# Kernel optimization log

Hardware: AMD Instinct MI355X
Metric: run time of the kernel (lower is better)

Reference implementation:

```python
import jax, jax.numpy as jnp
import numpy as np

B, T, H = 128, 1024, 512


def setup_inputs() -> dict:
    key = jax.random.key(0)
    ks = jax.random.split(key, 4)
    vel = jax.random.normal(ks[0], (B, T, 2), dtype=jnp.float32)
    # weight_ih ~ N(0, sqrt(1/2)); weight_hh orthogonal; biases zero; output zeroed
    # (we use random output weights so fwd output is non-trivial for testing)
    W_ih = jax.random.normal(ks[1], (H, 2), dtype=jnp.float32) * np.sqrt(0.5)
    A = jax.random.normal(ks[2], (H, H), dtype=jnp.float32)
    Q, _ = jnp.linalg.qr(A)
    W_hh = Q.astype(jnp.float32)
    b_ih = jnp.zeros((H,), dtype=jnp.float32)
    b_hh = jnp.zeros((H,), dtype=jnp.float32)
    W_out = jax.random.normal(ks[3], (2, H), dtype=jnp.float32) * 0.05
    b_out = jnp.zeros((2,), dtype=jnp.float32)
    return {"vel": vel, "W_ih": W_ih, "W_hh": W_hh, "b_ih": b_ih,
            "b_hh": b_hh, "W_out": W_out, "b_out": b_out}


def reference(vel, W_ih, W_hh, b_ih, b_hh, W_out, b_out):
    # Precompute input projection for all timesteps: [B, T, H]
    x_proj = jnp.einsum('btc,hc->bth', vel, W_ih) + b_ih + b_hh
    x_tbh = jnp.swapaxes(x_proj, 0, 1)  # [T, B, H] for scan over time

    def step(h, x_t):
        # h: [B, H]; x_t: [B, H]
        h_new = jnp.tanh(x_t + h @ W_hh.T)
        return h_new, h_new

    h0 = jnp.zeros((vel.shape[0], W_hh.shape[0]), dtype=vel.dtype)
    _, u_tbh = jax.lax.scan(step, h0, x_tbh)
    u_vals = jnp.swapaxes(u_tbh, 0, 1)  # [B, T, H]
    pos_est = jnp.einsum('bth,oh->bto', u_vals, W_out) + b_out  # [B, T, 2]
    return pos_est, u_vals
```

## Files before the change

kernel.cpp:

```cpp
#include <hip/hip_runtime.h>
#include <hip/hip_bf16.h>


#define TT 1024
#define BB 128
#define HH 512

typedef short s16x8 __attribute__((ext_vector_type(8)));
typedef float f32x4 __attribute__((ext_vector_type(4)));
typedef unsigned int uint;
typedef unsigned short ushort_t;
typedef unsigned long long u64;

#define MFMA_B16(a, b, c) __builtin_amdgcn_mfma_f32_16x16x32_bf16((a), (b), (c), 0, 0, 0)
#define ALD(p) __hip_atomic_load((p), __ATOMIC_RELAXED, __HIP_MEMORY_SCOPE_AGENT)
#define AST(p, v) __hip_atomic_store((p), (v), __ATOMIC_RELAXED, __HIP_MEMORY_SCOPE_AGENT)

static __device__ __forceinline__ ushort_t bf16_rne(float f) {
  uint u = __float_as_uint(f);
  u += 0x7fffu + ((u >> 16) & 1u);
  return (ushort_t)(u >> 16);
}

static __device__ __forceinline__ float tanh_fast(float z) {
  float e = __expf(2.0f * z);
  return 1.0f - 2.0f * __builtin_amdgcn_rcpf(e + 1.0f);
}

static __device__ __forceinline__ s16x8 packW(const float* wp) {
  float4 lo = *(const float4*)wp;
  float4 hi = *(const float4*)(wp + 4);
  s16x8 s;
  s[0] = (short)bf16_rne(lo.x); s[1] = (short)bf16_rne(lo.y);
  s[2] = (short)bf16_rne(lo.z); s[3] = (short)bf16_rne(lo.w);
  s[4] = (short)bf16_rne(hi.x); s[5] = (short)bf16_rne(hi.y);
  s[6] = (short)bf16_rne(hi.z); s[7] = (short)bf16_rne(hi.w);
  return s;
}

__global__ __launch_bounds__(256) void rnn_kernel(
    const float* __restrict__ vel, const float* __restrict__ W_ih,
    const float* __restrict__ W_hh, const float* __restrict__ b_ih,
    const float* __restrict__ b_hh, float* __restrict__ u_out,
    u64* __restrict__ pub) {
  __shared__ uint4 hlds_mem[2048];
  char* hlds = (char*)hlds_mem;

  const int tid = threadIdx.x;
  const int lane = tid & 63;
  const int w = tid >> 6;
  const int c = blockIdx.x & 7;
  const int p = blockIdx.x >> 3;
  const int l15 = lane & 15;
  const int kg = lane >> 4;
  const int n0 = p * 128 + w * 32;
  const uint swz = ((uint)l15 & 7u) << 4;

  s16x8 wl[2][4], wr[2][12];
#pragma unroll
  for (int nt = 0; nt < 2; ++nt) {
    const float* wb = W_hh + (size_t)(n0 + nt * 16 + l15) * HH + kg * 8;
#pragma unroll
    for (int kk = 0; kk < 4; ++kk)
      wl[nt][kk] = packW(wb + (p * 4 + kk) * 32);
#pragma unroll
    for (int j = 0; j < 12; ++j)
      wr[nt][j] = packW(wb + (((p * 4 + 4 + j) & 15)) * 32);
  }
  float wih0[2], wih1[2], bs[2];
#pragma unroll
  for (int nt = 0; nt < 2; ++nt) {
    int n = n0 + nt * 16 + l15;
    wih0[nt] = W_ih[n * 2 + 0];
    wih1[nt] = W_ih[n * 2 + 1];
    bs[nt] = b_ih[n] + b_hh[n];
  }

  {
    uint4 z = {0u, 0u, 0u, 0u};
    uint4* zp = (uint4*)(hlds + tid * 64);
    zp[0] = z; zp[1] = z; zp[2] = z; zp[3] = z;
  }
  __syncthreads();

  const f32x4 z4 = {0.f, 0.f, 0.f, 0.f};
  const int ps0 = (p + 1) & 3, ps1 = (p + 2) & 3, ps2 = (p + 3) & 3;
  const uint remoff = (uint)(p * 256 + 256);

  for (int t = 0; t < TT; ++t) {
    const int cur = t & 1;
    const int nxt = cur ^ 1;

    u64 g00 = 0, g01 = 0, g02 = 0, g03 = 0;
    u64 g10 = 0, g11 = 0, g12 = 0, g13 = 0;
    u64 g20 = 0, g21 = 0, g22 = 0, g23 = 0;
    const u64* sp0 = pub + ((size_t)(cur * 8 + c) * 4 + ps0) * 1024 + tid * 4;
    const u64* sp1 = pub + ((size_t)(cur * 8 + c) * 4 + ps1) * 1024 + tid * 4;
    const u64* sp2 = pub + ((size_t)(cur * 8 + c) * 4 + ps2) * 1024 + tid * 4;
    if (t > 0) {
      g00 = ALD(sp0); g01 = ALD(sp0 + 1); g02 = ALD(sp0 + 2); g03 = ALD(sp0 + 3);
      g10 = ALD(sp1); g11 = ALD(sp1 + 1); g12 = ALD(sp1 + 2); g13 = ALD(sp1 + 3);
      g20 = ALD(sp2); g21 = ALD(sp2 + 1); g22 = ALD(sp2 + 2); g23 = ALD(sp2 + 3);
      asm volatile("" ::: "memory");
    }

    float2 v[4];
#pragma unroll
    for (int r = 0; r < 4; ++r)
      v[r] = *(const float2*)(vel + ((size_t)(c * 16 + kg * 4 + r) * TT + t) * 2);

    f32x4 a00 = z4, a01 = z4, a10 = z4, a11 = z4;
    const uint abase = (uint)cur * 16384u + (uint)l15 * 1024u + (uint)kg * 16u;
#pragma unroll
    for (int kk = 0; kk < 4; ++kk) {
      s16x8 f = *(const s16x8*)(hlds + ((abase + (uint)(p * 256 + kk * 64)) ^ swz));
      if (kk & 1) { a01 = MFMA_B16(f, wl[0][kk], a01); a11 = MFMA_B16(f, wl[1][kk], a11); }
      else        { a00 = MFMA_B16(f, wl[0][kk], a00); a10 = MFMA_B16(f, wl[1][kk], a10); }
    }

    if (t > 0) {
      const uint tgt = (uint)t;
      const uint grow = (uint)tid >> 4;
      const uint gb = ((uint)cur * 16384u + grow * 1024u + (((uint)tid << 2) & 63u) * 4u) ^
                      ((grow & 7u) << 4);
      while (true) {
        uint mn = min(min((uint)(g00 >> 32), (uint)(g01 >> 32)),
                      min((uint)(g02 >> 32), (uint)(g03 >> 32)));
        if (mn >= tgt) break;
        g00 = ALD(sp0); g01 = ALD(sp0 + 1); g02 = ALD(sp0 + 2); g03 = ALD(sp0 + 3);
      }
      { uint4 d = {(uint)g00, (uint)g01, (uint)g02, (uint)g03};
        *(uint4*)(hlds + (gb ^ ((uint)ps0 * 256u))) = d; }
      while (true) {
        uint mn = min(min((uint)(g10 >> 32), (uint)(g11 >> 32)),
                      min((uint)(g12 >> 32), (uint)(g13 >> 32)));
        if (mn >= tgt) break;
        g10 = ALD(sp1); g11 = ALD(sp1 + 1); g12 = ALD(sp1 + 2); g13 = ALD(sp1 + 3);
      }
      { uint4 d = {(uint)g10, (uint)g11, (uint)g12, (uint)g13};
        *(uint4*)(hlds + (gb ^ ((uint)ps1 * 256u))) = d; }
      while (true) {
        uint mn = min(min((uint)(g20 >> 32), (uint)(g21 >> 32)),
                      min((uint)(g22 >> 32), (uint)(g23 >> 32)));
        if (mn >= tgt) break;
        g20 = ALD(sp2); g21 = ALD(sp2 + 1); g22 = ALD(sp2 + 2); g23 = ALD(sp2 + 3);
      }
      { uint4 d = {(uint)g20, (uint)g21, (uint)g22, (uint)g23};
        *(uint4*)(hlds + (gb ^ ((uint)ps2 * 256u))) = d; }
      __syncthreads();
    }

#pragma unroll
    for (int j = 0; j < 12; ++j) {
      uint off = (remoff + (uint)(j * 64)) & 1023u;
      s16x8 f = *(const s16x8*)(hlds + ((abase + off) ^ swz));
      if (j & 1) { a01 = MFMA_B16(f, wr[0][j], a01); a11 = MFMA_B16(f, wr[1][j], a11); }
      else       { a00 = MFMA_B16(f, wr[0][j], a00); a10 = MFMA_B16(f, wr[1][j], a10); }
    }
    f32x4 acc0 = a00 + a01;
    f32x4 acc1 = a10 + a11;

    float uv0[4], uv1[4];
    ushort_t hb0[4], hb1[4];
#pragma unroll
    for (int r = 0; r < 4; ++r) {
      float x0 = fmaf(v[r].x, wih0[0], fmaf(v[r].y, wih1[0], bs[0]));
      float x1 = fmaf(v[r].x, wih0[1], fmaf(v[r].y, wih1[1], bs[1]));
      uv0[r] = tanh_fast(x0 + acc0[r]);
      uv1[r] = tanh_fast(x1 + acc1[r]);
      hb0[r] = bf16_rne(uv0[r]);
      hb1[r] = bf16_rne(uv1[r]);
    }

    if (t < TT - 1) {
      const bool odd = (l15 & 1) != 0;
      const uint rowbase = (uint)(kg * 4) + (odd ? 2u : 0u);
      const uint cpq = (uint)(w * 16) + ((uint)l15 >> 1);
      u64* dpb = pub + ((size_t)(nxt * 8 + c) * 4 + p) * 1024;
      const u64 tagw = (u64)(uint)(t + 1) << 32;
      const uint ldsb = (uint)nxt * 16384u;
#pragma unroll
      for (int nt = 0; nt < 2; ++nt) {
        const ushort_t* hb = nt ? hb1 : hb0;
        uint a01p = (uint)hb[0] | ((uint)hb[1] << 16);
        uint a23p = (uint)hb[2] | ((uint)hb[3] << 16);
        uint b01p = __shfl_xor(a01p, 1);
        uint b23p = __shfl_xor(a23p, 1);
        uint eP = odd ? b23p : a01p;
        uint oP = odd ? a23p : b01p;
        uint pr0 = (eP & 0xFFFFu) | (oP << 16);
        uint pr1 = (eP >> 16) | (oP & 0xFFFF0000u);
        uint cp = cpq + (uint)(nt * 8);
        AST(dpb + rowbase * 64 + cp, (u64)pr0 | tagw);
        AST(dpb + (rowbase + 1) * 64 + cp, (u64)pr1 | tagw);
        uint cb = (uint)(n0 + nt * 16 + (l15 & ~1)) * 2u;
        *(uint*)(hlds + ((ldsb + rowbase * 1024u + cb) ^ ((rowbase & 7u) << 4))) = pr0;
        *(uint*)(hlds + ((ldsb + (rowbase + 1) * 1024u + cb) ^ (((rowbase + 1) & 7u) << 4))) = pr1;
      }
    }

#pragma unroll
    for (int r = 0; r < 4; ++r) {
      size_t ub = ((size_t)(c * 16 + kg * 4 + r) * TT + t) * HH;
      __builtin_nontemporal_store(uv0[r], u_out + ub + n0 + l15);
      __builtin_nontemporal_store(uv1[r], u_out + ub + n0 + 16 + l15);
    }

    if (t == TT - 1) break;
    __syncthreads();
  }
}

__global__ void init_kernel(u64* pub) {
  int idx = (blockIdx.x * 256 + threadIdx.x) * 4;
#pragma unroll
  for (int k = 0; k < 4; ++k)
    __hip_atomic_store(&pub[idx + k], 0ull, __ATOMIC_RELAXED, __HIP_MEMORY_SCOPE_AGENT);
}

__global__ __launch_bounds__(256) void pos_kernel(const float* __restrict__ u,
                                                  const float* __restrict__ W_out,
                                                  const float* __restrict__ b_out,
                                                  float* __restrict__ pos) {
  int row = blockIdx.x * 4 + (threadIdx.x >> 6);
  int lane = threadIdx.x & 63;
  const float* ur = u + (size_t)row * HH + lane * 8;
  float4 u0 = *(const float4*)ur;
  float4 u1 = *(const float4*)(ur + 4);
  float4 w00 = *(const float4*)(W_out + lane * 8);
  float4 w01 = *(const float4*)(W_out + lane * 8 + 4);
  float4 w10 = *(const float4*)(W_out + HH + lane * 8);
  float4 w11 = *(const float4*)(W_out + HH + lane * 8 + 4);
  float p0 = u0.x * w00.x + u0.y * w00.y + u0.z * w00.z + u0.w * w00.w +
             u1.x * w01.x + u1.y * w01.y + u1.z * w01.z + u1.w * w01.w;
  float p1 = u0.x * w10.x + u0.y * w10.y + u0.z * w10.z + u0.w * w10.w +
             u1.x * w11.x + u1.y * w11.y + u1.z * w11.z + u1.w * w11.w;
#pragma unroll
  for (int off = 32; off; off >>= 1) {
    p0 += __shfl_xor(p0, off);
    p1 += __shfl_xor(p1, off);
  }
  if (lane == 0) {
    pos[(size_t)row * 2 + 0] = p0 + b_out[0];
    pos[(size_t)row * 2 + 1] = p1 + b_out[1];
  }
}

extern "C" void kernel_launch(void* const* d_in, const int* in_sizes, int n_in,
                              void* d_out, int out_size, void* d_ws, size_t ws_size,
                              hipStream_t stream) {
  const float* vel   = (const float*)d_in[0];
  const float* W_ih  = (const float*)d_in[1];
  const float* W_hh  = (const float*)d_in[2];
  const float* b_ih  = (const float*)d_in[3];
  const float* b_hh  = (const float*)d_in[4];
  const float* W_out = (const float*)d_in[5];
  const float* b_out = (const float*)d_in[6];

  float* pos = (float*)d_out;
  float* u   = pos + (size_t)BB * TT * 2;

  u64* pub = (u64*)d_ws;

  init_kernel<<<64, 256, 0, stream>>>(pub);
  rnn_kernel<<<32, 256, 0, stream>>>(vel, W_ih, W_hh, b_ih, b_hh, u, pub);
  pos_kernel<<<(BB * TT) / 4, 256, 0, stream>>>(u, W_out, b_out, pos);
}
```

Measured before the change: 2.245 ms.

## Repartition RNN across 8 blocks of 512 threads, two batch chunks per block

The recurrent kernel previously split each 16-row batch chunk across 4 blocks, each owning 128 hidden units, and exchanged partial hidden states through tagged global memory every step. Now each block has 8 waves owning 256 hidden units and processes two batch chunks together. Each block therefore exchanges only with one partner block, and the two chunks share the same register-resident weight fragments, so each wait covers more MFMA work. The trade-off is fewer blocks in flight (8 instead of 32), more LDS per block, and higher register pressure from doubled accumulators.

After: 6.001 ms. 2.67x slower.

```diff
diff --git a/kernel.cpp b/kernel.cpp
--- a/kernel.cpp
+++ b/kernel.cpp
@@ -11,6 +11,7 @@
 typedef unsigned int uint;
 typedef unsigned short ushort_t;
 typedef unsigned long long u64;
+typedef uint u32x4 __attribute__((ext_vector_type(4)));
 
 #define MFMA_B16(a, b, c) __builtin_amdgcn_mfma_f32_16x16x32_bf16((a), (b), (c), 0, 0, 0)
 #define ALD(p) __hip_atomic_load((p), __ATOMIC_RELAXED, __HIP_MEMORY_SCOPE_AGENT)
@@ -38,34 +39,87 @@
   return s;
 }
 
-__global__ __launch_bounds__(256) void rnn_kernel(
+static __device__ __forceinline__ uint tagmin4(u64 a, u64 b, u64 c, u64 d) {
+  uint m0 = (uint)(a >> 32), m1 = (uint)(b >> 32);
+  uint m2 = (uint)(c >> 32), m3 = (uint)(d >> 32);
+  uint x = m0 < m1 ? m0 : m1;
+  uint y = m2 < m3 ? m2 : m3;
+  return x < y ? x : y;
+}
+
+#define EPI(cc, ldsoff, acc0, acc1, vv)                                          \
+  {                                                                              \
+    float uv0[4], uv1[4];                                                        \
+    ushort_t hb0v[4], hb1v[4];                                                   \
+    _Pragma("unroll") for (int r = 0; r < 4; ++r) {                              \
+      float x0 = fmaf(vv[r].x, wih0[0], fmaf(vv[r].y, wih1[0], bs[0]));          \
+      float x1 = fmaf(vv[r].x, wih0[1], fmaf(vv[r].y, wih1[1], bs[1]));          \
+      uv0[r] = tanh_fast(x0 + acc0[r]);                                          \
+      uv1[r] = tanh_fast(x1 + acc1[r]);                                          \
+      hb0v[r] = bf16_rne(uv0[r]);                                                \
+      hb1v[r] = bf16_rne(uv1[r]);                                                \
+    }                                                                            \
+    if (t < TT - 1) {                                                            \
+      const bool odd = (l15 & 1) != 0;                                           \
+      const uint rowbase = (uint)(kg * 4) + (odd ? 2u : 0u);                     \
+      u64* dpb = pub + ((size_t)(nxt * 8 + (cc)) * 2 + half) * 2048;             \
+      const u64 tw = (u64)(uint)(t + 1) << 32;                                   \
+      const uint ldsb = (uint)(ldsoff) + (uint)nxt * 16384u;                     \
+      _Pragma("unroll") for (int nt = 0; nt < 2; ++nt) {                         \
+        const ushort_t* hb = nt ? hb1v : hb0v;                                   \
+        uint a01p = (uint)hb[0] | ((uint)hb[1] << 16);                           \
+        uint a23p = (uint)hb[2] | ((uint)hb[3] << 16);                           \
+        uint b01p = __shfl_xor(a01p, 1);                                         \
+        uint b23p = __shfl_xor(a23p, 1);                                         \
+        uint eP = odd ? b23p : a01p;                                             \
+        uint oP = odd ? a23p : b01p;                                             \
+        uint pr0 = (eP & 0xFFFFu) | (oP << 16);                                  \
+        uint pr1 = (eP >> 16) | (oP & 0xFFFF0000u);                              \
+        uint cp = (uint)(w * 16) + ((uint)l15 >> 1) + (uint)(nt * 8);            \
+        AST(dpb + rowbase * 128 + cp, (u64)pr0 | tw);                            \
+        AST(dpb + (rowbase + 1) * 128 + cp, (u64)pr1 | tw);                      \
+        uint cb = (uint)(n0 + nt * 16 + (l15 & ~1)) * 2u;                        \
+        *(uint*)(hlds + ((ldsb + rowbase * 1024u + cb) ^                         \
+                         ((rowbase & 7u) << 4))) = pr0;                          \
+        *(uint*)(hlds + ((ldsb + (rowbase + 1) * 1024u + cb) ^                   \
+                         (((rowbase + 1) & 7u) << 4))) = pr1;                    \
+      }                                                                          \
+    }                                                                            \
+    _Pragma("unroll") for (int r = 0; r < 4; ++r) {                              \
+      size_t ub = ((size_t)((cc)*16 + kg * 4 + r) * TT + t) * HH;                \
+      __builtin_nontemporal_store(uv0[r], u_out + ub + n0 + l15);                \
+      __builtin_nontemporal_store(uv1[r], u_out + ub + n0 + 16 + l15);           \
+    }                                                                            \
+  }
+
+__global__ __launch_bounds__(512, 2) void rnn_kernel(
     const float* __restrict__ vel, const float* __restrict__ W_ih,
     const float* __restrict__ W_hh, const float* __restrict__ b_ih,
     const float* __restrict__ b_hh, float* __restrict__ u_out,
     u64* __restrict__ pub) {
-  __shared__ uint4 hlds_mem[2048];
+  __shared__ uint4 hlds_mem[4096];
   char* hlds = (char*)hlds_mem;
 
   const int tid = threadIdx.x;
   const int lane = tid & 63;
   const int w = tid >> 6;
-  const int c = blockIdx.x & 7;
-  const int p = blockIdx.x >> 3;
+  const int pr_ = blockIdx.x >> 1;
+  const int half = blockIdx.x & 1;
+  const int cA = pr_ * 2, cB = pr_ * 2 + 1;
   const int l15 = lane & 15;
   const int kg = lane >> 4;
-  const int n0 = p * 128 + w * 32;
+  const int n0 = half * 256 + w * 32;
   const uint swz = ((uint)l15 & 7u) << 4;
 
-  s16x8 wl[2][4], wr[2][12];
+  s16x8 wfr[2][16];
 #pragma unroll
   for (int nt = 0; nt < 2; ++nt) {
     const float* wb = W_hh + (size_t)(n0 + nt * 16 + l15) * HH + kg * 8;
 #pragma unroll
-    for (int kk = 0; kk < 4; ++kk)
-      wl[nt][kk] = packW(wb + (p * 4 + kk) * 32);
-#pragma unroll
-    for (int j = 0; j < 12; ++j)
-      wr[nt][j] = packW(wb + (((p * 4 + 4 + j) & 15)) * 32);
+    for (int q = 0; q < 16; ++q) {
+      int kt = (q < 8) ? (half * 8 + q) : ((1 - half) * 8 + (q - 8));
+      wfr[nt][q] = packW(wb + kt * 32);
+    }
   }
   float wih0[2], wih1[2], bs[2];
 #pragma unroll
@@ -78,133 +132,95 @@
 
   {
     uint4 z = {0u, 0u, 0u, 0u};
-    uint4* zp = (uint4*)(hlds + tid * 64);
-    zp[0] = z; zp[1] = z; zp[2] = z; zp[3] = z;
+#pragma unroll
+    for (int k = 0; k < 8; ++k) *(uint4*)(hlds + tid * 16 + k * 8192) = z;
   }
   __syncthreads();
 
   const f32x4 z4 = {0.f, 0.f, 0.f, 0.f};
-  const int ps0 = (p + 1) & 3, ps1 = (p + 2) & 3, ps2 = (p + 3) & 3;
-  const uint remoff = (uint)(p * 256 + 256);
+  const uint lbyte = (uint)half * 512u;
+  const uint rbyte = (uint)(1 - half) * 512u;
 
   for (int t = 0; t < TT; ++t) {
     const int cur = t & 1;
     const int nxt = cur ^ 1;
 
-    u64 g00 = 0, g01 = 0, g02 = 0, g03 = 0;
-    u64 g10 = 0, g11 = 0, g12 = 0, g13 = 0;
-    u64 g20 = 0, g21 = 0, g22 = 0, g23 = 0;
-    const u64* sp0 = pub + ((size_t)(cur * 8 + c) * 4 + ps0) * 1024 + tid * 4;
-    const u64* sp1 = pub + ((size_t)(cur * 8 + c) * 4 + ps1) * 1024 + tid * 4;
-    const u64* sp2 = pub + ((size_t)(cur * 8 + c) * 4 + ps2) * 1024 + tid * 4;
+    const u64* spA = pub + ((size_t)(cur * 8 + cA) * 2 + (1 - half)) * 2048 + tid * 4;
+    const u64* spB = pub + ((size_t)(cur * 8 + cB) * 2 + (1 - half)) * 2048 + tid * 4;
+    u64 gA0 = 0, gA1 = 0, gA2 = 0, gA3 = 0, gB0 = 0, gB1 = 0, gB2 = 0, gB3 = 0;
     if (t > 0) {
-      g00 = ALD(sp0); g01 = ALD(sp0 + 1); g02 = ALD(sp0 + 2); g03 = ALD(sp0 + 3);
-      g10 = ALD(sp1); g11 = ALD(sp1 + 1); g12 = ALD(sp1 + 2); g13 = ALD(sp1 + 3);
-      g20 = ALD(sp2); g21 = ALD(sp2 + 1); g22 = ALD(sp2 + 2); g23 = ALD(sp2 + 3);
-      asm volatile("" ::: "memory");
-    }
-
-    float2 v[4];
-#pragma unroll
-    for (int r = 0; r < 4; ++r)
-      v[r] = *(const float2*)(vel + ((size_t)(c * 16 + kg * 4 + r) * TT + t) * 2);
-
-    f32x4 a00 = z4, a01 = z4, a10 = z4, a11 = z4;
-    const uint abase = (uint)cur * 16384u + (uint)l15 * 1024u + (uint)kg * 16u;
-#pragma unroll
-    for (int kk = 0; kk < 4; ++kk) {
-      s16x8 f = *(const s16x8*)(hlds + ((abase + (uint)(p * 256 + kk * 64)) ^ swz));
-      if (kk & 1) { a01 = MFMA_B16(f, wl[0][kk], a01); a11 = MFMA_B16(f, wl[1][kk], a11); }
-      else        { a00 = MFMA_B16(f, wl[0][kk], a00); a10 = MFMA_B16(f, wl[1][kk], a10); }
+      gA0 = ALD(spA); gA1 = ALD(spA + 1); gA2 = ALD(spA + 2); gA3 = ALD(spA + 3);
+      gB0 = ALD(spB); gB1 = ALD(spB + 1); gB2 = ALD(spB + 2); gB3 = ALD(spB + 3);
+    }
+
+    float2 vA[4], vB[4];
+#pragma unroll
+    for (int r = 0; r < 4; ++r) {
+      vA[r] = *(const float2*)(vel + ((size_t)(cA * 16 + kg * 4 + r) * TT + t) * 2);
+      vB[r] = *(const float2*)(vel + ((size_t)(cB * 16 + kg * 4 + r) * TT + t) * 2);
+    }
+
+    f32x4 aA00 = z4, aA01 = z4, aA10 = z4, aA11 = z4;
+    f32x4 aB00 = z4, aB01 = z4, aB10 = z4, aB11 = z4;
+    const uint baseA = (uint)cur * 16384u + (uint)l15 * 1024u + (uint)kg * 16u;
+    const uint baseB = baseA + 32768u;
+#pragma unroll
+    for (int q = 0; q < 8; ++q) {
+      s16x8 fA = *(const s16x8*)(hlds + ((baseA + lbyte + (uint)q * 64u) ^ swz));
+      s16x8 fB = *(const s16x8*)(hlds + ((baseB + lbyte + (uint)q * 64u) ^ swz));
+      if (q & 1) {
+        aA01 = MFMA_B16(fA, wfr[0][q], aA01); aA11 = MFMA_B16(fA, wfr[1][q], aA11);
+        aB01 = MFMA_B16(fB, wfr[0][q], aB01); aB11 = MFMA_B16(fB, wfr[1][q], aB11);
+      } else {
+        aA00 = MFMA_B16(fA, wfr[0][q], aA00); aA10 = MFMA_B16(fA, wfr[1][q], aA10);
+        aB00 = MFMA_B16(fB, wfr[0][q], aB00); aB10 = MFMA_B16(fB, wfr[1][q], aB10);
+      }
     }
 
     if (t > 0) {
       const uint tgt = (uint)t;
-      const uint grow = (uint)tid >> 4;
-      const uint gb = ((uint)cur * 16384u + grow * 1024u + (((uint)tid << 2) & 63u) * 4u) ^
-                      ((grow & 7u) << 4);
-      while (true) {
-        uint mn = min(min((uint)(g00 >> 32), (uint)(g01 >> 32)),
-                      min((uint)(g02 >> 32), (uint)(g03 >> 32)));
-        if (mn >= tgt) break;
-        g00 = ALD(sp0); g01 = ALD(sp0 + 1); g02 = ALD(sp0 + 2); g03 = ALD(sp0 + 3);
-      }
-      { uint4 d = {(uint)g00, (uint)g01, (uint)g02, (uint)g03};
-        *(uint4*)(hlds + (gb ^ ((uint)ps0 * 256u))) = d; }
-      while (true) {
-        uint mn = min(min((uint)(g10 >> 32), (uint)(g11 >> 32)),
-                      min((uint)(g12 >> 32), (uint)(g13 >> 32)));
-        if (mn >= tgt) break;
-        g10 = ALD(sp1); g11 = ALD(sp1 + 1); g12 = ALD(sp1 + 2); g13 = ALD(sp1 + 3);
-      }
-      { uint4 d = {(uint)g10, (uint)g11, (uint)g12, (uint)g13};
-        *(uint4*)(hlds + (gb ^ ((uint)ps1 * 256u))) = d; }
-      while (true) {
-        uint mn = min(min((uint)(g20 >> 32), (uint)(g21 >> 32)),
-                      min((uint)(g22 >> 32), (uint)(g23 >> 32)));
-        if (mn >= tgt) break;
-        g20 = ALD(sp2); g21 = ALD(sp2 + 1); g22 = ALD(sp2 + 2); g23 = ALD(sp2 + 3);
-      }
-      { uint4 d = {(uint)g20, (uint)g21, (uint)g22, (uint)g23};
-        *(uint4*)(hlds + (gb ^ ((uint)ps2 * 256u))) = d; }
-      __syncthreads();
-    }
-
-#pragma unroll
-    for (int j = 0; j < 12; ++j) {
-      uint off = (remoff + (uint)(j * 64)) & 1023u;
-      s16x8 f = *(const s16x8*)(hlds + ((abase + off) ^ swz));
-      if (j & 1) { a01 = MFMA_B16(f, wr[0][j], a01); a11 = MFMA_B16(f, wr[1][j], a11); }
-      else       { a00 = MFMA_B16(f, wr[0][j], a00); a10 = MFMA_B16(f, wr[1][j], a10); }
-    }
-    f32x4 acc0 = a00 + a01;
-    f32x4 acc1 = a10 + a11;
-
-    float uv0[4], uv1[4];
-    ushort_t hb0[4], hb1[4];
-#pragma unroll
-    for (int r = 0; r < 4; ++r) {
-      float x0 = fmaf(v[r].x, wih0[0], fmaf(v[r].y, wih1[0], bs[0]));
-      float x1 = fmaf(v[r].x, wih0[1], fmaf(v[r].y, wih1[1], bs[1]));
-      uv0[r] = tanh_fast(x0 + acc0[r]);
-      uv1[r] = tanh_fast(x1 + acc1[r]);
-      hb0[r] = bf16_rne(uv0[r]);
-      hb1[r] = bf16_rne(uv1[r]);
-    }
-
-    if (t < TT - 1) {
-      const bool odd = (l15 & 1) != 0;
-      const uint rowbase = (uint)(kg * 4) + (odd ? 2u : 0u);
-      const uint cpq = (uint)(w * 16) + ((uint)l15 >> 1);
-      u64* dpb = pub + ((size_t)(nxt * 8 + c) * 4 + p) * 1024;
-      const u64 tagw = (u64)(uint)(t + 1) << 32;
-      const uint ldsb = (uint)nxt * 16384u;
-#pragma unroll
-      for (int nt = 0; nt < 2; ++nt) {
-        const ushort_t* hb = nt ? hb1 : hb0;
-        uint a01p = (uint)hb[0] | ((uint)hb[1] << 16);
-        uint a23p = (uint)hb[2] | ((uint)hb[3] << 16);
-        uint b01p = __shfl_xor(a01p, 1);
-        uint b23p = __shfl_xor(a23p, 1);
-        uint eP = odd ? b23p : a01p;
-        uint oP = odd ? a23p : b01p;
-        uint pr0 = (eP & 0xFFFFu) | (oP << 16);
-        uint pr1 = (eP >> 16) | (oP & 0xFFFF0000u);
-        uint cp = cpq + (uint)(nt * 8);
-        AST(dpb + rowbase * 64 + cp, (u64)pr0 | tagw);
-        AST(dpb + (rowbase + 1) * 64 + cp, (u64)pr1 | tagw);
-        uint cb = (uint)(n0 + nt * 16 + (l15 & ~1)) * 2u;
-        *(uint*)(hlds + ((ldsb + rowbase * 1024u + cb) ^ ((rowbase & 7u) << 4))) = pr0;
-        *(uint*)(hlds + ((ldsb + (rowbase + 1) * 1024u + cb) ^ (((rowbase + 1) & 7u) << 4))) = pr1;
-      }
-    }
-
-#pragma unroll
-    for (int r = 0; r < 4; ++r) {
-      size_t ub = ((size_t)(c * 16 + kg * 4 + r) * TT + t) * HH;
-      __builtin_nontemporal_store(uv0[r], u_out + ub + n0 + l15);
-      __builtin_nontemporal_store(uv1[r], u_out + ub + n0 + 16 + l15);
-    }
+      while (tagmin4(gA0, gA1, gA2, gA3) < tgt) {
+        gA0 = ALD(spA); gA1 = ALD(spA + 1); gA2 = ALD(spA + 2); gA3 = ALD(spA + 3);
+      }
+      asm volatile("" ::: "memory");
+      {
+        uint row = (uint)tid >> 5;
+        uint ab = ((uint)cur * 16384u + row * 1024u + rbyte + ((uint)tid & 31u) * 16u) ^
+                  ((row & 7u) << 4);
+        u32x4 dw = {(uint)gA0, (uint)gA1, (uint)gA2, (uint)gA3};
+        *(u32x4*)(hlds + ab) = dw;
+      }
+      while (tagmin4(gB0, gB1, gB2, gB3) < tgt) {
+        gB0 = ALD(spB); gB1 = ALD(spB + 1); gB2 = ALD(spB + 2); gB3 = ALD(spB + 3);
+      }
+      asm volatile("" ::: "memory");
+      {
+        uint row = (uint)tid >> 5;
+        uint ab = (32768u + (uint)cur * 16384u + row * 1024u + rbyte +
+                   ((uint)tid & 31u) * 16u) ^ ((row & 7u) << 4);
+        u32x4 dw = {(uint)gB0, (uint)gB1, (uint)gB2, (uint)gB3};
+        *(u32x4*)(hlds + ab) = dw;
+      }
+    }
+    __syncthreads();
+
+#pragma unroll
+    for (int q = 8; q < 16; ++q) {
+      s16x8 fA = *(const s16x8*)(hlds + ((baseA + rbyte + (uint)(q - 8) * 64u) ^ swz));
+      s16x8 fB = *(const s16x8*)(hlds + ((baseB + rbyte + (uint)(q - 8) * 64u) ^ swz));
+      if (q & 1) {
+        aA01 = MFMA_B16(fA, wfr[0][q], aA01); aA11 = MFMA_B16(fA, wfr[1][q], aA11);
+        aB01 = MFMA_B16(fB, wfr[0][q], aB01); aB11 = MFMA_B16(fB, wfr[1][q], aB11);
+      } else {
+        aA00 = MFMA_B16(fA, wfr[0][q], aA00); aA10 = MFMA_B16(fA, wfr[1][q], aA10);
+        aB00 = MFMA_B16(fB, wfr[0][q], aB00); aB10 = MFMA_B16(fB, wfr[1][q], aB10);
+      }
+    }
+    f32x4 accA0 = aA00 + aA01, accA1 = aA10 + aA11;
+    f32x4 accB0 = aB00 + aB01, accB1 = aB10 + aB11;
+
+    EPI(cA, 0, accA0, accA1, vA);
+    EPI(cB, 32768, accB0, accB1, vB);
 
     if (t == TT - 1) break;
     __syncthreads();
@@ -212,10 +228,8 @@
 }
 
 __global__ void init_kernel(u64* pub) {
-  int idx = (blockIdx.x * 256 + threadIdx.x) * 4;
-#pragma unroll
-  for (int k = 0; k < 4; ++k)
-    __hip_atomic_store(&pub[idx + k], 0ull, __ATOMIC_RELAXED, __HIP_MEMORY_SCOPE_AGENT);
+  size_t idx = (size_t)blockIdx.x * 256 + threadIdx.x;
+  __hip_atomic_store(&pub[idx], 0ull, __ATOMIC_RELAXED, __HIP_MEMORY_SCOPE_AGENT);
 }
 
 __global__ __launch_bounds__(256) void pos_kernel(const float* __restrict__ u,
@@ -262,7 +276,7 @@
 
   u64* pub = (u64*)d_ws;
 
-  init_kernel<<<64, 256, 0, stream>>>(pub);
-  rnn_kernel<<<32, 256, 0, stream>>>(vel, W_ih, W_hh, b_ih, b_hh, u, pub);
+  init_kernel<<<256, 256, 0, stream>>>(pub);
+  rnn_kernel<<<8, 512, 0, stream>>>(vel, W_ih, W_hh, b_ih, b_hh, u, pub);
   pos_kernel<<<(BB * TT) / 4, 256, 0, stream>>>(u, W_out, b_out, pos);
 }
```
